# Kernel optimization log

Measured on AMD Instinct MI355X. Metric: run time of the kernel, lower is better.

Reference implementation:

```python
import jax, jax.numpy as jnp
import numpy as np

NUM_SEGMENTS_PER_PC = 100  # matches fill_max of box_ids_of_pts


def setup_inputs() -> dict:
    key = jax.random.key(0)
    k1, k2, k3 = jax.random.split(key, 3)
    B, C, N = 8, 128, 65536
    point_features = jax.random.normal(k1, (B, C, N), dtype=jnp.float32)
    points = jax.random.normal(k2, (B, N, 4), dtype=jnp.float32)
    box_ids_of_pts = jax.random.randint(k3, (B, N), 0, NUM_SEGMENTS_PER_PC, dtype=jnp.int64)
    return {"point_features": point_features, "points": points, "box_ids_of_pts": box_ids_of_pts}


def reference(point_features, points, box_ids_of_pts):
    # point_features: (B, C, N); box_ids_of_pts: (B, N) in {-1, 0..S-1}
    B, C, N = point_features.shape
    S = NUM_SEGMENTS_PER_PC
    # (B, N, C) -> flat (B*N, C) point features
    feats = jnp.transpose(point_features, (0, 2, 1)).reshape(B * N, C)
    labels = box_ids_of_pts.reshape(B * N)
    pc_idx = jnp.repeat(jnp.arange(B), N)
    # global segment id; label == -1 points routed to a dummy trailing bucket
    seg = jnp.where(labels >= 0, pc_idx * S + labels, B * S).astype(jnp.int32)
    # fused segment max-pool (replaces the per-unique-label max_pool1d loop)
    all_seg_feats = jax.ops.segment_max(feats, seg, num_segments=B * S + 1)[: B * S]
    # pretext_head_feats: (B*S, C), rows ordered by (pc_idx, sorted segment label),
    # identical ordering to the np.unique loop in the torch module.
    return all_seg_feats
```

## Files before the change

### kernel.cpp

```cpp
#include <hip/hip_runtime.h>

#define SEGS 100
#define C_TILE 4
#define BLOCK 1024
#define CHUNK 8192

__device__ __forceinline__ unsigned enc_f32(float f) {
    unsigned u = __float_as_uint(f);
    return u ^ (unsigned)(((int)u >> 31) | 0x80000000);
}
__device__ __forceinline__ float dec_f32(unsigned u) {
    unsigned m = (u & 0x80000000u) ? 0x80000000u : 0xFFFFFFFFu;
    return __uint_as_float(u ^ m);
}

__global__ __launch_bounds__(BLOCK) void seg_max_kernel(
    const float* __restrict__ pf,
    const int* __restrict__ labels,
    float* __restrict__ out,
    int C, int N)
{
    __shared__ unsigned acc[C_TILE * SEGS];
    __shared__ int lab[CHUNK];

    const int tid = threadIdx.x;
    const int tiles_per_b = C / C_TILE;
    const int b = blockIdx.x / tiles_per_b;
    const int c_base = (blockIdx.x % tiles_per_b) * C_TILE;

    for (int i = tid; i < C_TILE * SEGS; i += BLOCK) acc[i] = 0x007FFFFFu;

    const int wave  = tid >> 6;
    const int lane  = tid & 63;
    const int cl    = wave & (C_TILE - 1);
    const int strip = wave >> 2;
    const int c     = c_base + cl;

    const float4* pf4  = (const float4*)(pf + ((size_t)b * C + c) * (size_t)N);
    const int*    labg = labels + (size_t)b * N;
    unsigned*     accc = acc + cl * SEGS;

    const int it_per_chunk = CHUNK / 4 / 256;

    for (int chunk0 = 0; chunk0 < N; chunk0 += CHUNK) {
        __syncthreads();
        {
            const int4* src = (const int4*)(labg + chunk0);
            int4* dst = (int4*)lab;
            dst[tid]        = src[tid];
            dst[tid + 1024] = src[tid + 1024];
        }
        __syncthreads();

        #pragma unroll
        for (int it = 0; it < it_per_chunk; ++it) {
            int idx4 = it * 256 + strip * 64 + lane;
            float4 f = pf4[(chunk0 >> 2) + idx4];
            int4 l4  = ((const int4*)lab)[idx4];
            if ((unsigned)l4.x < SEGS) atomicMax(&accc[l4.x], enc_f32(f.x));
            if ((unsigned)l4.y < SEGS) atomicMax(&accc[l4.y], enc_f32(f.y));
            if ((unsigned)l4.z < SEGS) atomicMax(&accc[l4.z], enc_f32(f.z));
            if ((unsigned)l4.w < SEGS) atomicMax(&accc[l4.w], enc_f32(f.w));
        }
    }

    __syncthreads();
    if (tid < C_TILE * SEGS) {
        int ocl = tid & (C_TILE - 1);
        int l   = tid >> 2;
        float v = dec_f32(acc[ocl * SEGS + l]);
        out[((size_t)(b * SEGS + l)) * C + c_base + ocl] = v;
    }
}

extern "C" void kernel_launch(void* const* d_in, const int* in_sizes, int n_in,
                              void* d_out, int out_size, void* d_ws, size_t ws_size,
                              hipStream_t stream) {
    const float* pf    = (const float*)d_in[0];
    const int*   lab   = (const int*)d_in[2];
    float*       out   = (float*)d_out;

    const long long bn = in_sizes[2];
    const int C = (int)(in_sizes[0] / bn);
    const int B = out_size / (SEGS * C);
    const int N = (int)(bn / B);

    const int blocks = B * (C / C_TILE);
    seg_max_kernel<<<blocks, BLOCK, 0, stream>>>(pf, lab, out, C, N);
}
```

Measured before the change: 365.0 us.

## Split N across blocks and merge partial maxima with global atomics

```diff
diff --git a/kernel.cpp b/kernel.cpp
--- a/kernel.cpp
+++ b/kernel.cpp
@@ -1,7 +1,8 @@
 #include <hip/hip_runtime.h>
 
 #define SEGS 100
-#define C_TILE 4
+#define C_TILE 8
+#define NSPLIT 4
 #define BLOCK 1024
 #define CHUNK 8192
 
@@ -14,10 +15,23 @@
     return __uint_as_float(u ^ m);
 }
 
-__global__ __launch_bounds__(BLOCK) void seg_max_kernel(
+__global__ void init_kernel(unsigned* __restrict__ o, int n) {
+    int i = blockIdx.x * blockDim.x + threadIdx.x;
+    if (i < n) o[i] = 0x007FFFFFu;
+}
+
+__global__ void decode_kernel(unsigned* __restrict__ o, int n) {
+    int i = blockIdx.x * blockDim.x + threadIdx.x;
+    if (i < n) {
+        float f = dec_f32(o[i]);
+        ((float*)o)[i] = f;
+    }
+}
+
+__global__ __launch_bounds__(BLOCK) void seg_max_main(
     const float* __restrict__ pf,
     const int* __restrict__ labels,
-    float* __restrict__ out,
+    unsigned* __restrict__ outenc,
     int C, int N)
 {
     __shared__ unsigned acc[C_TILE * SEGS];
@@ -25,24 +39,27 @@
 
     const int tid = threadIdx.x;
     const int tiles_per_b = C / C_TILE;
-    const int b = blockIdx.x / tiles_per_b;
-    const int c_base = (blockIdx.x % tiles_per_b) * C_TILE;
+    int t = blockIdx.x;
+    const int split  = t % NSPLIT;  t /= NSPLIT;
+    const int c_tile = t % tiles_per_b; t /= tiles_per_b;
+    const int b = t;
 
     for (int i = tid; i < C_TILE * SEGS; i += BLOCK) acc[i] = 0x007FFFFFu;
 
     const int wave  = tid >> 6;
     const int lane  = tid & 63;
-    const int cl    = wave & (C_TILE - 1);
-    const int strip = wave >> 2;
-    const int c     = c_base + cl;
+    const int cl    = wave >> 1;
+    const int strip = wave & 1;
+    const int c     = c_tile * C_TILE + cl;
 
-    const float4* pf4  = (const float4*)(pf + ((size_t)b * C + c) * (size_t)N);
-    const int*    labg = labels + (size_t)b * N;
+    const int npart = N / NSPLIT;
+    const int nbase = split * npart;
+
+    const float4* pf4  = (const float4*)(pf + ((size_t)b * C + c) * (size_t)N + nbase);
+    const int*    labg = labels + (size_t)b * N + nbase;
     unsigned*     accc = acc + cl * SEGS;
 
-    const int it_per_chunk = CHUNK / 4 / 256;
-
-    for (int chunk0 = 0; chunk0 < N; chunk0 += CHUNK) {
+    for (int chunk0 = 0; chunk0 < npart; chunk0 += CHUNK) {
         __syncthreads();
         {
             const int4* src = (const int4*)(labg + chunk0);
@@ -53,8 +70,8 @@
         __syncthreads();
 
         #pragma unroll
-        for (int it = 0; it < it_per_chunk; ++it) {
-            int idx4 = it * 256 + strip * 64 + lane;
+        for (int it = 0; it < CHUNK / 4 / 128; ++it) {
+            int idx4 = it * 128 + strip * 64 + lane;
             float4 f = pf4[(chunk0 >> 2) + idx4];
             int4 l4  = ((const int4*)lab)[idx4];
             if ((unsigned)l4.x < SEGS) atomicMax(&accc[l4.x], enc_f32(f.x));
@@ -67,24 +84,29 @@
     __syncthreads();
     if (tid < C_TILE * SEGS) {
         int ocl = tid & (C_TILE - 1);
-        int l   = tid >> 2;
-        float v = dec_f32(acc[ocl * SEGS + l]);
-        out[((size_t)(b * SEGS + l)) * C + c_base + ocl] = v;
+        int l   = tid >> 3;
+        atomicMax(&outenc[((size_t)(b * SEGS + l)) * C + c_tile * C_TILE + ocl],
+                  acc[ocl * SEGS + l]);
     }
 }
 
 extern "C" void kernel_launch(void* const* d_in, const int* in_sizes, int n_in,
                               void* d_out, int out_size, void* d_ws, size_t ws_size,
                               hipStream_t stream) {
-    const float* pf    = (const float*)d_in[0];
-    const int*   lab   = (const int*)d_in[2];
-    float*       out   = (float*)d_out;
+    const float* pf  = (const float*)d_in[0];
+    const int*   lab = (const int*)d_in[2];
+    unsigned*    oe  = (unsigned*)d_out;
 
     const long long bn = in_sizes[2];
     const int C = (int)(in_sizes[0] / bn);
     const int B = out_size / (SEGS * C);
     const int N = (int)(bn / B);
 
-    const int blocks = B * (C / C_TILE);
-    seg_max_kernel<<<blocks, BLOCK, 0, stream>>>(pf, lab, out, C, N);
+    const int init_blocks = (out_size + 1023) / 1024;
+    init_kernel<<<init_blocks, 1024, 0, stream>>>(oe, out_size);
+
+    const int blocks = B * (C / C_TILE) * NSPLIT;
+    seg_max_main<<<blocks, BLOCK, 0, stream>>>(pf, lab, oe, C, N);
+
+    decode_kernel<<<init_blocks, 1024, 0, stream>>>(oe, out_size);
 }
```

New measurement: 371.9 us. Within noise of the previous version (+1.9%).
